# Performance work log

Hardware: AMD Instinct MI355X
Metric: run time of the kernel (lower is better)

Reference implementation:

```python
import jax, jax.numpy as jnp
import numpy as np

D_MODEL = 512


def _xavier(key, shape, gain=1.0):
    fan_in, fan_out = shape[1], shape[0]
    a = gain * np.sqrt(6.0 / (fan_in + fan_out))
    return jax.random.uniform(key, shape, jnp.float32, -a, a)


def setup_inputs() -> dict:
    key = jax.random.key(0)
    kx, kq, kk, kv, ko = jax.random.split(key, 5)
    x = jax.random.normal(kx, (16, D_MODEL, 32, 32), jnp.float32)
    Wq = _xavier(kq, (D_MODEL, D_MODEL))
    Wk = _xavier(kk, (D_MODEL, D_MODEL))
    Wv = _xavier(kv, (D_MODEL, D_MODEL))
    Wo = _xavier(ko, (D_MODEL, D_MODEL), gain=1e-05)
    bq = jnp.zeros((D_MODEL,), jnp.float32)
    bk = jnp.zeros((D_MODEL,), jnp.float32)
    bv = jnp.zeros((D_MODEL,), jnp.float32)
    bo = jnp.zeros((D_MODEL,), jnp.float32)
    return {"x": x, "Wq": Wq, "bq": bq, "Wk": Wk, "bk": bk, "Wv": Wv, "bv": bv, "Wo": Wo, "bo": bo}


def _proj_tokens(x, W, b):
    # 1x1 conv == channel matmul, then flatten spatial to tokens: [B, H*W, C]
    B, C, H, Wd = x.shape
    y = jnp.einsum('bchw,oc->bhwo', x, W) + b  # [B, H, W, C_out]
    return y.reshape(B, H * Wd, -1)


def reference(x, Wq, bq, Wk, bk, Wv, bv, Wo, bo):
    B, C, H, W = x.shape
    temperature = jnp.asarray(C, x.dtype) ** 0.5
    q = _proj_tokens(x, Wq, bq)  # [B, N, C]
    k = _proj_tokens(x, Wk, bk)
    v = _proj_tokens(x, Wv, bv)
    scores = jnp.einsum('bnc,bmc->bnm', q / temperature, k)  # [B, N, N]
    attention = jax.nn.softmax(scores, axis=-1)
    out = jnp.einsum('bnm,bmc->bnc', attention, v)  # [B, N, C]
    out = out.reshape(B, H, W, C)
    out = jnp.einsum('bhwc,oc->bohw', out, Wo) + bo[None, :, None, None]
    return (x + out, attention)
```

## Files before the change

kernel.cpp:

```cpp
#include <hip/hip_runtime.h>
#include <hip/hip_bf16.h>

#define DM 512
#define NTOK 1024
#define NB 16

typedef _Float16 f16;
typedef _Float16 half8 __attribute__((ext_vector_type(8)));
typedef _Float16 half4_t __attribute__((ext_vector_type(4)));
typedef float f32x4 __attribute__((ext_vector_type(4)));

__device__ __forceinline__ void gload16(const void* g, void* l) {
    __builtin_amdgcn_global_load_lds(
        (const __attribute__((address_space(1))) void*)g,
        (__attribute__((address_space(3))) void*)l, 16, 0, 0);
}

__global__ __launch_bounds__(256)
void transpose_x_kernel(const float* __restrict__ x, f16* __restrict__ xt) {
    __shared__ float tile[32][33];
    int b = blockIdx.z;
    int n0 = blockIdx.x * 32, c0 = blockIdx.y * 32;
    int tx = threadIdx.x, ty = threadIdx.y;
    const float* xb = x + (size_t)b * DM * NTOK;
#pragma unroll
    for (int i = 0; i < 32; i += 8)
        tile[ty + i][tx] = xb[(size_t)(c0 + ty + i) * NTOK + n0 + tx];
    __syncthreads();
    f16* xtb = xt + (size_t)b * NTOK * DM;
#pragma unroll
    for (int i = 0; i < 32; i += 8)
        xtb[(size_t)(n0 + ty + i) * DM + c0 + tx] = (f16)tile[tx][ty + i];
}

__global__ __launch_bounds__(256)
void convert_wqkv_kernel(const float* __restrict__ Wq, const float* __restrict__ Wk,
                         const float* __restrict__ Wv, const float* __restrict__ bq,
                         const float* __restrict__ bk, const float* __restrict__ bv,
                         f16* __restrict__ dst, float* __restrict__ bdst) {
    int i = blockIdx.x * 256 + threadIdx.x;
    int row = i >> 9, col = i & 511;
    float v = (row < 512) ? Wq[i] : (row < 1024) ? Wk[(row - 512) * 512 + col]
                                                 : Wv[(row - 1024) * 512 + col];
    dst[i] = (f16)v;
    if (i < 1536)
        bdst[i] = (i < 512) ? bq[i] : (i < 1024) ? bk[i - 512] : bv[i - 1024];
}

__global__ __launch_bounds__(256)
void convert_w_kernel(const float* __restrict__ src, f16* __restrict__ dst, int n) {
    int i = blockIdx.x * 256 + threadIdx.x;
    if (i < n) dst[i] = (f16)src[i];
}

__global__ __launch_bounds__(256)
void transpose_v_kernel(const f16* __restrict__ vtok, f16* __restrict__ vh) {
    __shared__ f16 tile[32][34];
    int b = blockIdx.z;
    int n0 = blockIdx.x * 32, c0 = blockIdx.y * 32;
    int tx = threadIdx.x, ty = threadIdx.y;
    const f16* src = vtok + (size_t)b * NTOK * DM;
#pragma unroll
    for (int i = 0; i < 32; i += 8)
        tile[ty + i][tx] = src[(size_t)(n0 + ty + i) * DM + c0 + tx];
    __syncthreads();
    f16* dst = vh + (size_t)b * DM * NTOK;
#pragma unroll
    for (int i = 0; i < 32; i += 8)
        dst[(size_t)(c0 + ty + i) * NTOK + n0 + tx] = tile[tx][ty + i];
}

template<int MODE, int KC>
__global__ __launch_bounds__(256)
void gemm_nt(const f16* __restrict__ A, const f16* __restrict__ B, void* __restrict__ Cout,
             const float* __restrict__ bias, const float* __restrict__ resid,
             f16* __restrict__ aux, float* __restrict__ rowsum,
             int ldA, int ldB, int ldC,
             long sA, long sB, long sC, long sR, float scale) {
    __shared__ f16 As[128 * 32];
    __shared__ f16 Bs[128 * 32];
    int z = blockIdx.z;
    const f16* Ab = A + (size_t)z * sA;
    const f16* Bb = B + (size_t)z * sB;
    int tid = threadIdx.x;
    int wave = tid >> 6, lane = tid & 63;
    int wr = wave >> 1, wc = wave & 1;
    int tI = blockIdx.y * 128, tJ = blockIdx.x * 128;

    f32x4 acc[4][4];
#pragma unroll
    for (int m = 0; m < 4; ++m)
#pragma unroll
        for (int n = 0; n < 4; ++n) acc[m][n] = (f32x4){0.f, 0.f, 0.f, 0.f};

    int frow = lane & 15, fk = (lane >> 4) * 8;
    int sr = lane >> 2, sc = (lane & 3) * 8;

    for (int k0 = 0; k0 < KC; k0 += 32) {
#pragma unroll
        for (int h = 0; h < 2; ++h) {
            int chunk = wave * 2 + h;
            int r = chunk * 16 + sr;
            const f16* ga = Ab + (size_t)(tI + r) * ldA + k0 + sc;
            const f16* gb = Bb + (size_t)(tJ + r) * ldB + k0 + sc;
            gload16(ga, &As[chunk * 512 + lane * 8]);
            gload16(gb, &Bs[chunk * 512 + lane * 8]);
        }
        asm volatile("s_waitcnt vmcnt(0)" ::: "memory");
        __syncthreads();

        half8 af[4], bf[4];
#pragma unroll
        for (int m = 0; m < 4; ++m)
            af[m] = *(const half8*)&As[(wr * 64 + m * 16 + frow) * 32 + fk];
#pragma unroll
        for (int n = 0; n < 4; ++n)
            bf[n] = *(const half8*)&Bs[(wc * 64 + n * 16 + frow) * 32 + fk];
#pragma unroll
        for (int m = 0; m < 4; ++m)
#pragma unroll
            for (int n = 0; n < 4; ++n)
                acc[m][n] = __builtin_amdgcn_mfma_f32_16x16x32_f16(af[m], bf[n], acc[m][n], 0, 0, 0);
        __syncthreads();
    }

    int ro = (lane >> 4) * 4, co = lane & 15;
#pragma unroll
    for (int m = 0; m < 4; ++m) {
#pragma unroll
        for (int r = 0; r < 4; ++r) {
            int gi = tI + wr * 64 + m * 16 + ro + r;
            float rs = 0.f, inv = 0.f;
            if (MODE == 5) inv = 1.0f / rowsum[z * 1024 + gi];
#pragma unroll
            for (int n = 0; n < 4; ++n) {
                int gj = tJ + wc * 64 + n * 16 + co;
                float v = acc[m][n][r];
                if (MODE == 0) {
                    v += bias[gj];
                    if (gj < 1024)
                        ((f16*)Cout)[(size_t)z * sC + (size_t)gi * ldC + gj] = (f16)v;
                    else
                        aux[(size_t)z * 524288 + (size_t)gi * 512 + (gj - 1024)] = (f16)v;
                } else if (MODE == 2) {
                    float e = __expf(fminf(v * scale, 14.f) - 4.f);
                    ((f16*)Cout)[((size_t)z * 1024 + gi) * 2048 + 1024 + gj] = (f16)e;
                    rs += e;
                } else if (MODE == 3) {
                    ((float*)Cout)[(size_t)z * sC + (size_t)gi * ldC + gj] =
                        v + bias[gi] + resid[(size_t)z * sR + (size_t)gi * ldC + gj];
                } else {
                    ((f16*)Cout)[(size_t)z * sC + (size_t)gi * ldC + gj] = (f16)(v * inv);
                }
            }
            if (MODE == 2) {
                rs += __shfl_xor(rs, 1, 16);
                rs += __shfl_xor(rs, 2, 16);
                rs += __shfl_xor(rs, 4, 16);
                rs += __shfl_xor(rs, 8, 16);
                if ((lane & 15) == 0) atomicAdd(&rowsum[z * 1024 + gi], rs);
            }
        }
    }
}

__global__ __launch_bounds__(256)
void finalize_attn(float* __restrict__ attn, const float* __restrict__ rowsum) {
    size_t row = blockIdx.x;
    float inv = 1.0f / rowsum[row];
    float* prow = attn + row * 1024;
    half4_t h = *(const half4_t*)((const f16*)prow + 1024 + threadIdx.x * 4);
    __syncthreads();
    float4 o = {(float)h[0] * inv, (float)h[1] * inv, (float)h[2] * inv, (float)h[3] * inv};
    ((float4*)prow)[threadIdx.x] = o;
}

extern "C" void kernel_launch(void* const* d_in, const int* in_sizes, int n_in,
                              void* d_out, int out_size, void* d_ws, size_t ws_size,
                              hipStream_t stream) {
    const float* x  = (const float*)d_in[0];
    const float* Wq = (const float*)d_in[1];
    const float* bq = (const float*)d_in[2];
    const float* Wk = (const float*)d_in[3];
    const float* bk = (const float*)d_in[4];
    const float* Wv = (const float*)d_in[5];
    const float* bv = (const float*)d_in[6];
    const float* Wo = (const float*)d_in[7];
    const float* bo = (const float*)d_in[8];

    float* out0 = (float*)d_out;
    float* attn = (float*)d_out + (size_t)NB * DM * NTOK;

    f16* ws    = (f16*)d_ws;
    f16* xt    = ws;
    f16* oh    = ws;
    f16* qk    = ws + 8388608;
    f16* vh    = ws + 25165824;
    f16* wqkvh = ws + 33554432;
    f16* woh   = ws + 33554432;
    float* bqkv   = (float*)(ws + 34340864);
    float* rowsum = (float*)(ws + 34343936);

    f16* vtok = (f16*)out0;

    const long sTok   = (long)NTOK * DM;
    const long sQK    = (long)NTOK * 1024;
    const long sEslot = (long)NTOK * 2048;
    const float scal = 0.044194173824159216f;

    hipMemsetAsync(rowsum, 0, 16384 * sizeof(float), stream);
    transpose_x_kernel<<<dim3(32, 16, NB), dim3(32, 8), 0, stream>>>(x, xt);
    convert_wqkv_kernel<<<3072, 256, 0, stream>>>(Wq, Wk, Wv, bq, bk, bv, wqkvh, bqkv);

    gemm_nt<0, 512><<<dim3(12, 8, NB), 256, 0, stream>>>(xt, wqkvh, qk, bqkv, nullptr,
        vtok, nullptr, 512, 512, 1024, sTok, 0, sQK, 0, 0.f);

    convert_w_kernel<<<1024, 256, 0, stream>>>(Wo, woh, 262144);
    transpose_v_kernel<<<dim3(32, 16, NB), dim3(32, 8), 0, stream>>>(vtok, vh);

    gemm_nt<2, 512><<<dim3(8, 8, NB), 256, 0, stream>>>(qk, qk + 512, attn, nullptr, nullptr,
        nullptr, rowsum, 1024, 1024, 0, sQK, sQK, 0, 0, scal);

    gemm_nt<5, 1024><<<dim3(4, 8, NB), 256, 0, stream>>>((const f16*)attn + 1024, vh, oh,
        nullptr, nullptr, nullptr, rowsum, 2048, 1024, 512, sEslot, sTok, sTok, 0, 0.f);

    finalize_attn<<<NB * NTOK, 256, 0, stream>>>(attn, rowsum);

    gemm_nt<3, 512><<<dim3(8, 4, NB), 256, 0, stream>>>(woh, oh, out0, bo, x,
        nullptr, nullptr, 512, 512, 1024, 0, sTok, sTok, sTok, 0.f);
}
```

Before: 184.6 us.

## Widen GEMM K-tile with XOR-swizzled LDS, vectorize transposes, fold memset into kernel

The GEMM now stages a 64-wide K slice per iteration, which halves the number of barriers and loop trips. Its LDS layout is XOR-swizzled to avoid bank conflicts on the fragment reads. The two transpose kernels switch to vector loads and stores (float4/half4) with a 8x32 thread shape. The rowsum memset is folded into the weight-conversion kernel to drop one launch. Doubling the LDS use may lower occupancy.

```diff
diff --git a/kernel.cpp b/kernel.cpp
--- a/kernel.cpp
+++ b/kernel.cpp
@@ -22,22 +22,22 @@
     int b = blockIdx.z;
     int n0 = blockIdx.x * 32, c0 = blockIdx.y * 32;
     int tx = threadIdx.x, ty = threadIdx.y;
-    const float* xb = x + (size_t)b * DM * NTOK;
-#pragma unroll
-    for (int i = 0; i < 32; i += 8)
-        tile[ty + i][tx] = xb[(size_t)(c0 + ty + i) * NTOK + n0 + tx];
+    const float* xb = x + (size_t)b * DM * NTOK + (size_t)(c0 + ty) * NTOK + n0 + tx * 4;
+    float4 v = *(const float4*)xb;
+    tile[ty][tx * 4 + 0] = v.x; tile[ty][tx * 4 + 1] = v.y;
+    tile[ty][tx * 4 + 2] = v.z; tile[ty][tx * 4 + 3] = v.w;
     __syncthreads();
-    f16* xtb = xt + (size_t)b * NTOK * DM;
-#pragma unroll
-    for (int i = 0; i < 32; i += 8)
-        xtb[(size_t)(n0 + ty + i) * DM + c0 + tx] = (f16)tile[tx][ty + i];
+    half4_t h = {(f16)tile[tx * 4 + 0][ty], (f16)tile[tx * 4 + 1][ty],
+                 (f16)tile[tx * 4 + 2][ty], (f16)tile[tx * 4 + 3][ty]};
+    *(half4_t*)&xt[(size_t)b * NTOK * DM + (size_t)(n0 + ty) * DM + c0 + tx * 4] = h;
 }
 
 __global__ __launch_bounds__(256)
 void convert_wqkv_kernel(const float* __restrict__ Wq, const float* __restrict__ Wk,
                          const float* __restrict__ Wv, const float* __restrict__ bq,
                          const float* __restrict__ bk, const float* __restrict__ bv,
-                         f16* __restrict__ dst, float* __restrict__ bdst) {
+                         f16* __restrict__ dst, float* __restrict__ bdst,
+                         float* __restrict__ rowsum) {
     int i = blockIdx.x * 256 + threadIdx.x;
     int row = i >> 9, col = i & 511;
     float v = (row < 512) ? Wq[i] : (row < 1024) ? Wk[(row - 512) * 512 + col]
@@ -45,6 +45,7 @@
     dst[i] = (f16)v;
     if (i < 1536)
         bdst[i] = (i < 512) ? bq[i] : (i < 1024) ? bk[i - 512] : bv[i - 1024];
+    if (blockIdx.x < 64) rowsum[blockIdx.x * 256 + threadIdx.x] = 0.f;
 }
 
 __global__ __launch_bounds__(256)
@@ -55,19 +56,18 @@
 
 __global__ __launch_bounds__(256)
 void transpose_v_kernel(const f16* __restrict__ vtok, f16* __restrict__ vh) {
-    __shared__ f16 tile[32][34];
+    __shared__ f16 tile[32][36];
     int b = blockIdx.z;
     int n0 = blockIdx.x * 32, c0 = blockIdx.y * 32;
     int tx = threadIdx.x, ty = threadIdx.y;
-    const f16* src = vtok + (size_t)b * NTOK * DM;
-#pragma unroll
-    for (int i = 0; i < 32; i += 8)
-        tile[ty + i][tx] = src[(size_t)(n0 + ty + i) * DM + c0 + tx];
+    const f16* src = vtok + (size_t)b * NTOK * DM + (size_t)(n0 + ty) * DM + c0 + tx * 4;
+    half4_t v = *(const half4_t*)src;
+    tile[ty][tx * 4 + 0] = v[0]; tile[ty][tx * 4 + 1] = v[1];
+    tile[ty][tx * 4 + 2] = v[2]; tile[ty][tx * 4 + 3] = v[3];
     __syncthreads();
-    f16* dst = vh + (size_t)b * DM * NTOK;
-#pragma unroll
-    for (int i = 0; i < 32; i += 8)
-        dst[(size_t)(c0 + ty + i) * NTOK + n0 + tx] = tile[tx][ty + i];
+    half4_t h = {tile[tx * 4 + 0][ty], tile[tx * 4 + 1][ty],
+                 tile[tx * 4 + 2][ty], tile[tx * 4 + 3][ty]};
+    *(half4_t*)&vh[(size_t)b * DM * NTOK + (size_t)(c0 + ty) * NTOK + n0 + tx * 4] = h;
 }
 
 template<int MODE, int KC>
@@ -77,8 +77,8 @@
              f16* __restrict__ aux, float* __restrict__ rowsum,
              int ldA, int ldB, int ldC,
              long sA, long sB, long sC, long sR, float scale) {
-    __shared__ f16 As[128 * 32];
-    __shared__ f16 Bs[128 * 32];
+    __shared__ f16 As[128 * 64];
+    __shared__ f16 Bs[128 * 64];
     int z = blockIdx.z;
     const f16* Ab = A + (size_t)z * sA;
     const f16* Bb = B + (size_t)z * sB;
@@ -93,34 +93,40 @@
 #pragma unroll
         for (int n = 0; n < 4; ++n) acc[m][n] = (f32x4){0.f, 0.f, 0.f, 0.f};
 
-    int frow = lane & 15, fk = (lane >> 4) * 8;
-    int sr = lane >> 2, sc = (lane & 3) * 8;
-
-    for (int k0 = 0; k0 < KC; k0 += 32) {
-#pragma unroll
-        for (int h = 0; h < 2; ++h) {
-            int chunk = wave * 2 + h;
-            int r = chunk * 16 + sr;
-            const f16* ga = Ab + (size_t)(tI + r) * ldA + k0 + sc;
-            const f16* gb = Bb + (size_t)(tJ + r) * ldB + k0 + sc;
-            gload16(ga, &As[chunk * 512 + lane * 8]);
-            gload16(gb, &Bs[chunk * 512 + lane * 8]);
+    int frow = lane & 15, fks = lane >> 4;
+
+    for (int k0 = 0; k0 < KC; k0 += 64) {
+#pragma unroll
+        for (int h = 0; h < 4; ++h) {
+            int L = h * 256 + tid;
+            int r = L >> 3;
+            int gc = ((L & 7) ^ (r & 7)) * 8;
+            gload16(Ab + (size_t)(tI + r) * ldA + k0 + gc, &As[L * 8]);
+            gload16(Bb + (size_t)(tJ + r) * ldB + k0 + gc, &Bs[L * 8]);
         }
         asm volatile("s_waitcnt vmcnt(0)" ::: "memory");
         __syncthreads();
 
-        half8 af[4], bf[4];
-#pragma unroll
-        for (int m = 0; m < 4; ++m)
-            af[m] = *(const half8*)&As[(wr * 64 + m * 16 + frow) * 32 + fk];
-#pragma unroll
-        for (int n = 0; n < 4; ++n)
-            bf[n] = *(const half8*)&Bs[(wc * 64 + n * 16 + frow) * 32 + fk];
-#pragma unroll
-        for (int m = 0; m < 4; ++m)
-#pragma unroll
-            for (int n = 0; n < 4; ++n)
-                acc[m][n] = __builtin_amdgcn_mfma_f32_16x16x32_f16(af[m], bf[n], acc[m][n], 0, 0, 0);
+#pragma unroll
+        for (int ks = 0; ks < 2; ++ks) {
+            half8 af[4], bf[4];
+            int s = ks * 4 + fks;
+#pragma unroll
+            for (int m = 0; m < 4; ++m) {
+                int R = wr * 64 + m * 16 + frow;
+                af[m] = *(const half8*)&As[R * 64 + ((s ^ (R & 7)) << 3)];
+            }
+#pragma unroll
+            for (int n = 0; n < 4; ++n) {
+                int R = wc * 64 + n * 16 + frow;
+                bf[n] = *(const half8*)&Bs[R * 64 + ((s ^ (R & 7)) << 3)];
+            }
+#pragma unroll
+            for (int m = 0; m < 4; ++m)
+#pragma unroll
+                for (int n = 0; n < 4; ++n)
+                    acc[m][n] = __builtin_amdgcn_mfma_f32_16x16x32_f16(af[m], bf[n], acc[m][n], 0, 0, 0);
+        }
         __syncthreads();
     }
 
@@ -208,15 +214,14 @@
     const long sEslot = (long)NTOK * 2048;
     const float scal = 0.044194173824159216f;
 
-    hipMemsetAsync(rowsum, 0, 16384 * sizeof(float), stream);
-    transpose_x_kernel<<<dim3(32, 16, NB), dim3(32, 8), 0, stream>>>(x, xt);
-    convert_wqkv_kernel<<<3072, 256, 0, stream>>>(Wq, Wk, Wv, bq, bk, bv, wqkvh, bqkv);
+    transpose_x_kernel<<<dim3(32, 16, NB), dim3(8, 32), 0, stream>>>(x, xt);
+    convert_wqkv_kernel<<<3072, 256, 0, stream>>>(Wq, Wk, Wv, bq, bk, bv, wqkvh, bqkv, rowsum);
 
     gemm_nt<0, 512><<<dim3(12, 8, NB), 256, 0, stream>>>(xt, wqkvh, qk, bqkv, nullptr,
         vtok, nullptr, 512, 512, 1024, sTok, 0, sQK, 0, 0.f);
 
     convert_w_kernel<<<1024, 256, 0, stream>>>(Wo, woh, 262144);
-    transpose_v_kernel<<<dim3(32, 16, NB), dim3(32, 8), 0, stream>>>(vtok, vh);
+    transpose_v_kernel<<<dim3(32, 16, NB), dim3(8, 32), 0, stream>>>(vtok, vh);
 
     gemm_nt<2, 512><<<dim3(8, 8, NB), 256, 0, stream>>>(qk, qk + 512, attn, nullptr, nullptr,
         nullptr, rowsum, 1024, 1024, 0, sQK, sQK, 0, 0, scal);
```

New measurement: 171.7 us. 7.0% less time.
